# Kernel optimization log

Hardware: AMD Instinct MI355X
Metric: run time of the kernel (lower is better)

## Reference

```python
import jax, jax.numpy as jnp
import numpy as np


def setup_inputs() -> dict:
    key = jax.random.key(0)
    k1, k2, k3 = jax.random.split(key, 3)
    B, C, H, W = 8, 512, 32, 32
    x = jax.random.normal(k1, (B, C, H, W), dtype=jnp.float32)
    # Conv2d(ch, ch, 3, 1, 1) weights, PyTorch OIHW layout
    fan_in = C * 3 * 3
    weight = jax.random.normal(k2, (C, C, 3, 3), dtype=jnp.float32) / np.sqrt(fan_in)
    bias = jax.random.normal(k3, (C,), dtype=jnp.float32) * 0.01
    return {"x": x, "weight": weight, "bias": bias}


def reference(x, weight, bias):
    up = jnp.repeat(jnp.repeat(x, 2, axis=2), 2, axis=3)
    # Conv3x3, stride 1, padding 1 (same spatial size)
    out = jax.lax.conv_general_dilated(
        up, weight,
        window_strides=(1, 1),
        padding=((1, 1), (1, 1)),
        dimension_numbers=("NCHW", "OIHW", "NCHW"),
    )
    return out + bias[None, :, None, None]
```

## Files before the change

kernel.cpp:

```cpp
#include <hip/hip_runtime.h>
#include <hip/hip_bf16.h>
#include <stdint.h>


typedef __attribute__((ext_vector_type(8)))  __bf16 bf16x8;
typedef __attribute__((ext_vector_type(4)))  float  f32x4;
typedef __attribute__((ext_vector_type(4)))  int    int4v;

__device__ __forceinline__ void async16(const void* g, void* l) {
  __builtin_amdgcn_global_load_lds(
      (const __attribute__((address_space(1))) void*)g,
      (__attribute__((address_space(3))) void*)l,
      16, 0, 0);
}

__global__ void prep_weff(const float* __restrict__ w,
                          __hip_bfloat16* __restrict__ weff) {
  const int idx = blockIdx.x * 256 + threadIdx.x;
  const int co = idx >> 9;
  const int ci = idx & 511;
  const float* wp = w + (size_t)idx * 9;
  float t[9];
#pragma unroll
  for (int i = 0; i < 9; ++i) t[i] = wp[i];
#pragma unroll
  for (int py = 0; py < 2; ++py) {
#pragma unroll
    for (int px = 0; px < 2; ++px) {
      const int p = py * 2 + px;
#pragma unroll
      for (int ky = 0; ky < 2; ++ky) {
        const int ulo = (ky == 0) ? 0 : (py == 0 ? 1 : 2);
        const int uhi = (ky == 0) ? (py == 0 ? 0 : 1) : 2;
#pragma unroll
        for (int kx = 0; kx < 2; ++kx) {
          const int vlo = (kx == 0) ? 0 : (px == 0 ? 1 : 2);
          const int vhi = (kx == 0) ? (px == 0 ? 0 : 1) : 2;
          float s = 0.f;
          for (int u = ulo; u <= uhi; ++u)
            for (int v = vlo; v <= vhi; ++v)
              s += t[u * 3 + v];
          const int kk = ky * 2 + kx;
          weff[(((size_t)p * 512 + co) * 4 + kk) * 512 + ci] = __float2bfloat16(s);
        }
      }
    }
  }
}

__global__ void prep_xpad(const float* __restrict__ x,
                          __hip_bfloat16* __restrict__ xpad) {
  const int blk = blockIdx.x;
  const int cib = blk & 7;
  const int r   = (blk >> 3) & 31;
  const int b   = blk >> 8;
  const int tid = threadIdx.x;
  __shared__ __align__(16) __hip_bfloat16 ldsT[32][80];
  const int ci_l = tid >> 2;
  const int wq   = tid & 3;
  const float* xp = x + (((size_t)(b * 512 + cib * 64 + ci_l) * 32 + r) * 32) + wq * 8;
  float4 v0 = *(const float4*)(xp);
  float4 v1 = *(const float4*)(xp + 4);
  const int wb = wq * 8;
  ldsT[wb + 0][ci_l] = __float2bfloat16(v0.x);
  ldsT[wb + 1][ci_l] = __float2bfloat16(v0.y);
  ldsT[wb + 2][ci_l] = __float2bfloat16(v0.z);
  ldsT[wb + 3][ci_l] = __float2bfloat16(v0.w);
  ldsT[wb + 4][ci_l] = __float2bfloat16(v1.x);
  ldsT[wb + 5][ci_l] = __float2bfloat16(v1.y);
  ldsT[wb + 6][ci_l] = __float2bfloat16(v1.z);
  ldsT[wb + 7][ci_l] = __float2bfloat16(v1.w);
  __syncthreads();
  const int w_o = tid >> 3;
  const int ch  = tid & 7;
  char* dst = (char*)xpad +
      ((((size_t)(b * 34 + (r + 1)) * 34) + (w_o + 1)) * 512 + cib * 64 + ch * 8) * 2;
  *(int4v*)dst = *(const int4v*)&ldsT[w_o][ch * 8];
}

#define MM(a, b, c) __builtin_amdgcn_mfma_f32_16x16x32_bf16((a), (b), (c), 0, 0, 0)
#define BAR() asm volatile("s_barrier" ::: "memory")
#define PRIO(x) __builtin_amdgcn_s_setprio(x)
#define GATE(N) asm volatile("s_waitcnt vmcnt(" N ")" ::: "memory")

#define ST_A(T, h, d) do {                                                     \
    char* _l = lds + (d) * 32768 + (h) * 16384 + dA;                           \
    const __hip_bfloat16* _g = ((h) ? pA1 : pA0) + (size_t)(T) * 64;           \
    async16(_g, _l); async16(_g + 131072, _l + 8192); } while (0)

#define OFFB(T) (((((T) >> 4) * 34) + (((T) >> 3) & 1)) * 512 + ((T) & 7) * 64)
#define ST_B(T, h, d) do {                                                     \
    char* _l = lds + 65536 + (d) * 32768 + (h) * 16384 + dA;                   \
    const int _o = OFFB(T);                                                    \
    async16(((h) ? pB10 : pB00) + _o, _l);                                     \
    async16(((h) ? pB11 : pB01) + _o, _l + 8192); } while (0)

#define RD_A(D, S, mb) do {                                                    \
    _Pragma("unroll") for (int _m = 0; _m < 4; ++_m) {                         \
      (D)[_m * 2]     = *(const bf16x8*)((S) + ((mb) + _m) * 2048 + aoff0);    \
      (D)[_m * 2 + 1] = *(const bf16x8*)((S) + ((mb) + _m) * 2048 + aoff1); }  \
  } while (0)

#define RD_B(D, S, nb) do {                                                    \
    _Pragma("unroll") for (int _n = 0; _n < 2; ++_n) {                         \
      (D)[_n * 2]     = *(const bf16x8*)((S) + ((nb) + _n) * 2048 + aoff0);    \
      (D)[_n * 2 + 1] = *(const bf16x8*)((S) + ((nb) + _n) * 2048 + aoff1); }  \
  } while (0)

#define MFMAQ(mb, nb, A, B) do {                                               \
    _Pragma("unroll") for (int _m = 0; _m < 4; ++_m)                           \
      _Pragma("unroll") for (int _n = 0; _n < 2; ++_n) {                       \
        acc[(mb)+_m][(nb)+_n] = MM((A)[_m*2],   (B)[_n*2],   acc[(mb)+_m][(nb)+_n]); \
        acc[(mb)+_m][(nb)+_n] = MM((A)[_m*2+1], (B)[_n*2+1], acc[(mb)+_m][(nb)+_n]); } \
  } while (0)

#define ITER(T, SE, SM, S7, G3, G7) do {                                       \
                                                            \
  RD_A(A0, aS0, 0); RD_B(Bf, bS0, 0); if (SE) ST_A((T)+1, 1, 1);               \
  PRIO(1); MFMAQ(0, 0, A0, Bf); PRIO(0);                                       \
  RD_A(A1, aS0, 4); if (SE) ST_B((T)+1, 0, 1);                                 \
  PRIO(1); MFMAQ(4, 0, A1, Bf); PRIO(0);                                       \
  BAR();                                                                       \
                                                            \
  RD_B(Bf, bS0, 2); if (SE) ST_B((T)+1, 1, 1);                                 \
  PRIO(1); MFMAQ(4, 2, A1, Bf); PRIO(0);                                       \
  if (SM) ST_A((T)+2, 0, 0);                                                   \
  PRIO(1); MFMAQ(0, 2, A0, Bf); PRIO(0);                                       \
  GATE(G3); BAR();                                                             \
                                                            \
  RD_A(A0, aS1, 0); RD_B(Bf, bS1, 0); if (SM) ST_A((T)+2, 1, 0);               \
  PRIO(1); MFMAQ(0, 0, A0, Bf); PRIO(0);                                       \
  RD_A(A1, aS1, 4); if (SM) ST_B((T)+2, 0, 0);                                 \
  PRIO(1); MFMAQ(4, 0, A1, Bf); PRIO(0);                                       \
  BAR();                                                                       \
                                                            \
  RD_B(Bf, bS1, 2); if (SM) ST_B((T)+2, 1, 0);                                 \
  PRIO(1); MFMAQ(4, 2, A1, Bf); PRIO(0);                                       \
  if (S7) ST_A((T)+3, 0, 1);                                                   \
  PRIO(1); MFMAQ(0, 2, A0, Bf); PRIO(0);                                       \
  GATE(G7); BAR();                                                             \
} while (0)

__global__ __launch_bounds__(512, 2) void upconv_gemm(
    const __hip_bfloat16* __restrict__ xpad,
    const __hip_bfloat16* __restrict__ weff,
    const float* __restrict__ bias,
    float* __restrict__ out) {
  extern __shared__ __align__(16) char lds[];

  const int bid = blockIdx.x;
  const int g = bid & 7, i = bid >> 3;
  const int py = g >> 2;
  const int mt = (g >> 1) & 1;
  const int nh = g & 1;
  const int px = i & 1;
  const int nt = nh * 16 + (i >> 1);
  const int p  = py * 2 + px;
  const int co0 = mt << 8;
  const int n0  = nt << 8;
  const int b   = n0 >> 10;
  const int rb  = (n0 & 1023) >> 5;

  const int tid  = threadIdx.x;
  const int lane = tid & 63;
  const int wv   = tid >> 6;
  const int wr   = wv >> 2;
  const int wc   = wv & 3;

  const int srow = tid >> 3;
  const int sl   = (tid & 7) ^ (srow & 7);
  const int dA   = wv * 1024;

  const __hip_bfloat16* wpp = weff + ((size_t)p << 20);
  const __hip_bfloat16* pA0 = wpp + (size_t)(co0 + srow) * 2048 + sl * 8;
  const __hip_bfloat16* pA1 = pA0 + (size_t)128 * 2048;
  const __hip_bfloat16* pB00 = xpad +
      ((size_t)(b * 34 + rb + (srow >> 5) + py) * 34 + (srow & 31) + px) * 512 + sl * 8;
  const __hip_bfloat16* pB01 = xpad +
      ((size_t)(b * 34 + rb + ((64 + srow) >> 5) + py) * 34 + ((64 + srow) & 31) + px) * 512 + sl * 8;
  const __hip_bfloat16* pB10 = xpad +
      ((size_t)(b * 34 + rb + ((128 + srow) >> 5) + py) * 34 + ((128 + srow) & 31) + px) * 512 + sl * 8;
  const __hip_bfloat16* pB11 = xpad +
      ((size_t)(b * 34 + rb + ((192 + srow) >> 5) + py) * 34 + ((192 + srow) & 31) + px) * 512 + sl * 8;

  const int aoff0 = (lane & 15) * 128 + (((lane >> 4) ^ (lane & 7)) * 16);
  const int aoff1 = (lane & 15) * 128 + ((((lane >> 4) + 4) ^ (lane & 7)) * 16);
  const char* aS0 = lds + wr * 16384;
  const char* aS1 = aS0 + 32768;
  const char* bS0 = lds + 65536 + (wc >> 1) * 16384 + (wc & 1) * 8192;
  const char* bS1 = bS0 + 32768;

  f32x4 acc[8][4] = {};
  bf16x8 A0[8], A1[8], Bf[4];

  ST_A(0, 0, 0); ST_A(0, 1, 0); ST_B(0, 0, 0); ST_B(0, 1, 0);
  ST_A(1, 0, 1); ST_A(1, 1, 1); ST_B(1, 0, 1); ST_B(1, 1, 1);
  GATE("8"); BAR();

  ITER(0, false, true, true, "2", "2");
#pragma unroll 1
  for (int t = 2; t <= 28; t += 2) ITER(t, true, true, true, "2", "2");
  ITER(30, true, false, false, "0", "0");

#pragma unroll
  for (int m = 0; m < 8; ++m) {
    const int coB = co0 + wr * 128 + m * 16 + ((lane >> 4) << 2);
    float bv[4];
#pragma unroll
    for (int j = 0; j < 4; ++j) bv[j] = bias[coB + j];
#pragma unroll
    for (int nn = 0; nn < 4; ++nn) {
      const int nl = wc * 64 + nn * 16 + (lane & 15);
      const int rr = rb + (nl >> 5);
      const int ss = nl & 31;
      const int oh = rr * 2 + py;
      const int ow = ss * 2 + px;
      float* op = out + (((size_t)(b * 512 + coB) << 6) + oh) * 64 + ow;
#pragma unroll
      for (int j = 0; j < 4; ++j)
        op[(size_t)j * 4096] = acc[m][nn][j] + bv[j];
    }
  }
}

extern "C" void kernel_launch(void* const* d_in, const int* in_sizes, int n_in,
                              void* d_out, int out_size, void* d_ws, size_t ws_size,
                              hipStream_t stream) {
  (void)in_sizes; (void)n_in; (void)out_size; (void)ws_size;
  const float* x  = (const float*)d_in[0];
  const float* w  = (const float*)d_in[1];
  const float* bs = (const float*)d_in[2];
  float* out = (float*)d_out;
  char* ws = (char*)d_ws;
  __hip_bfloat16* xpad = (__hip_bfloat16*)ws;
  __hip_bfloat16* weff = (__hip_bfloat16*)(ws + (10u << 20));
  hipMemsetAsync(xpad, 0, (size_t)8 * 34 * 34 * 512 * 2, stream);
  prep_weff<<<dim3(1024), dim3(256), 0, stream>>>(w, weff);
  prep_xpad<<<dim3(2048), dim3(256), 0, stream>>>(x, xpad);
  upconv_gemm<<<dim3(256), dim3(512), 131072, stream>>>(xpad, weff, bs, out);
}
```

Baseline: 89.05 us.

## Double-buffer register fragments and coarsen global-to-LDS staging per barrier phase

Restructures the main loop so A and B fragments are double-buffered in registers (Aa/Ab, Ba/Bb), with LDS reads for the next quarter issued ahead of the MFMAs that consume the current one. Global-to-LDS async loads are merged into one A and one B issue per k-step instead of split halves, which changes the vmcnt gate values. The B pointers are now derived from a single base by fixed row offsets. The aim is to hide LDS read latency behind MFMAs, at the cost of more VGPRs, which could hurt occupancy at two blocks per CU.

New measurement: 84.26 us. 1.06x faster.

```diff
diff --git a/kernel.cpp b/kernel.cpp
--- a/kernel.cpp
+++ b/kernel.cpp
@@ -83,17 +83,20 @@
 #define PRIO(x) __builtin_amdgcn_s_setprio(x)
 #define GATE(N) asm volatile("s_waitcnt vmcnt(" N ")" ::: "memory")
 
-#define ST_A(T, h, d) do {                                                     \
-    char* _l = lds + (d) * 32768 + (h) * 16384 + dA;                           \
-    const __hip_bfloat16* _g = ((h) ? pA1 : pA0) + (size_t)(T) * 64;           \
-    async16(_g, _l); async16(_g + 131072, _l + 8192); } while (0)
+#define ST_A(T, d) do {                                                        \
+    char* _l = lds + (d) * 32768 + dA;                                         \
+    const __hip_bfloat16* _g = pA0 + (size_t)(T) * 64;                         \
+    async16(_g, _l); async16(_g + 131072, _l + 8192);                          \
+    async16(_g + 262144, _l + 16384); async16(_g + 393216, _l + 24576);        \
+  } while (0)
 
 #define OFFB(T) (((((T) >> 4) * 34) + (((T) >> 3) & 1)) * 512 + ((T) & 7) * 64)
-#define ST_B(T, h, d) do {                                                     \
-    char* _l = lds + 65536 + (d) * 32768 + (h) * 16384 + dA;                   \
+#define ST_B(T, d) do {                                                        \
+    char* _l = lds + 65536 + (d) * 32768 + dA;                                 \
     const int _o = OFFB(T);                                                    \
-    async16(((h) ? pB10 : pB00) + _o, _l);                                     \
-    async16(((h) ? pB11 : pB01) + _o, _l + 8192); } while (0)
+    async16(pB00 + _o, _l); async16(pB01 + _o, _l + 8192);                     \
+    async16(pB10 + _o, _l + 16384); async16(pB11 + _o, _l + 24576);            \
+  } while (0)
 
 #define RD_A(D, S, mb) do {                                                    \
     _Pragma("unroll") for (int _m = 0; _m < 4; ++_m) {                         \
@@ -114,31 +117,31 @@
         acc[(mb)+_m][(nb)+_n] = MM((A)[_m*2+1], (B)[_n*2+1], acc[(mb)+_m][(nb)+_n]); } \
   } while (0)
 
-#define ITER(T, SE, SM, S7, G3, G7) do {                                       \
-                                                            \
-  RD_A(A0, aS0, 0); RD_B(Bf, bS0, 0); if (SE) ST_A((T)+1, 1, 1);               \
-  PRIO(1); MFMAQ(0, 0, A0, Bf); PRIO(0);                                       \
-  RD_A(A1, aS0, 4); if (SE) ST_B((T)+1, 0, 1);                                 \
-  PRIO(1); MFMAQ(4, 0, A1, Bf); PRIO(0);                                       \
+#define ITER(T, SE, SO, GE, GO, LAST) do {                                     \
+                                                         \
+  RD_A(Ab, aS0, 4);                                                            \
+  PRIO(1); MFMAQ(0, 0, Aa, Ba); PRIO(0);                                       \
+  RD_B(Bb, bS0, 2);                                                            \
+  PRIO(1); MFMAQ(4, 0, Ab, Ba); PRIO(0);                                       \
   BAR();                                                                       \
-                                                            \
-  RD_B(Bf, bS0, 2); if (SE) ST_B((T)+1, 1, 1);                                 \
-  PRIO(1); MFMAQ(4, 2, A1, Bf); PRIO(0);                                       \
-  if (SM) ST_A((T)+2, 0, 0);                                                   \
-  PRIO(1); MFMAQ(0, 2, A0, Bf); PRIO(0);                                       \
-  GATE(G3); BAR();                                                             \
-                                                            \
-  RD_A(A0, aS1, 0); RD_B(Bf, bS1, 0); if (SM) ST_A((T)+2, 1, 0);               \
-  PRIO(1); MFMAQ(0, 0, A0, Bf); PRIO(0);                                       \
-  RD_A(A1, aS1, 4); if (SM) ST_B((T)+2, 0, 0);                                 \
-  PRIO(1); MFMAQ(4, 0, A1, Bf); PRIO(0);                                       \
+  if (SE) ST_A((T) + 2, 0);                                                    \
+  PRIO(1); MFMAQ(4, 2, Ab, Bb); PRIO(0);                                       \
+  GATE(GE); BAR();                                                             \
+  RD_A(Ab, aS1, 0); RD_B(Ba, bS1, 0);                                          \
+  if (SE) ST_B((T) + 2, 0);                                                    \
+  PRIO(1); MFMAQ(0, 2, Aa, Bb); PRIO(0);                                       \
+                                                          \
+  RD_A(Aa, aS1, 4);                                                            \
+  PRIO(1); MFMAQ(0, 0, Ab, Ba); PRIO(0);                                       \
+  RD_B(Bb, bS1, 2);                                                            \
+  PRIO(1); MFMAQ(4, 0, Aa, Ba); PRIO(0);                                       \
   BAR();                                                                       \
-                                                            \
-  RD_B(Bf, bS1, 2); if (SM) ST_B((T)+2, 1, 0);                                 \
-  PRIO(1); MFMAQ(4, 2, A1, Bf); PRIO(0);                                       \
-  if (S7) ST_A((T)+3, 0, 1);                                                   \
-  PRIO(1); MFMAQ(0, 2, A0, Bf); PRIO(0);                                       \
-  GATE(G7); BAR();                                                             \
+  if (SO) ST_A((T) + 3, 1);                                                    \
+  PRIO(1); MFMAQ(4, 2, Aa, Bb); PRIO(0);                                       \
+  GATE(GO); BAR();                                                             \
+  if (!LAST) { RD_A(Aa, aS0, 0); RD_B(Ba, bS0, 0); }                           \
+  if (SO) ST_B((T) + 3, 1);                                                    \
+  PRIO(1); MFMAQ(0, 2, Ab, Bb); PRIO(0);                                       \
 } while (0)
 
 __global__ __launch_bounds__(512, 2) void upconv_gemm(
@@ -173,15 +176,11 @@
 
   const __hip_bfloat16* wpp = weff + ((size_t)p << 20);
   const __hip_bfloat16* pA0 = wpp + (size_t)(co0 + srow) * 2048 + sl * 8;
-  const __hip_bfloat16* pA1 = pA0 + (size_t)128 * 2048;
   const __hip_bfloat16* pB00 = xpad +
       ((size_t)(b * 34 + rb + (srow >> 5) + py) * 34 + (srow & 31) + px) * 512 + sl * 8;
-  const __hip_bfloat16* pB01 = xpad +
-      ((size_t)(b * 34 + rb + ((64 + srow) >> 5) + py) * 34 + ((64 + srow) & 31) + px) * 512 + sl * 8;
-  const __hip_bfloat16* pB10 = xpad +
-      ((size_t)(b * 34 + rb + ((128 + srow) >> 5) + py) * 34 + ((128 + srow) & 31) + px) * 512 + sl * 8;
-  const __hip_bfloat16* pB11 = xpad +
-      ((size_t)(b * 34 + rb + ((192 + srow) >> 5) + py) * 34 + ((192 + srow) & 31) + px) * 512 + sl * 8;
+  const __hip_bfloat16* pB01 = pB00 + (size_t)2 * 34 * 512;
+  const __hip_bfloat16* pB10 = pB00 + (size_t)4 * 34 * 512;
+  const __hip_bfloat16* pB11 = pB00 + (size_t)6 * 34 * 512;
 
   const int aoff0 = (lane & 15) * 128 + (((lane >> 4) ^ (lane & 7)) * 16);
   const int aoff1 = (lane & 15) * 128 + ((((lane >> 4) + 4) ^ (lane & 7)) * 16);
@@ -191,16 +190,16 @@
   const char* bS1 = bS0 + 32768;
 
   f32x4 acc[8][4] = {};
-  bf16x8 A0[8], A1[8], Bf[4];
-
-  ST_A(0, 0, 0); ST_A(0, 1, 0); ST_B(0, 0, 0); ST_B(0, 1, 0);
-  ST_A(1, 0, 1); ST_A(1, 1, 1); ST_B(1, 0, 1); ST_B(1, 1, 1);
+  bf16x8 Aa[8], Ab[8], Ba[4], Bb[4];
+
+  ST_A(0, 0); ST_B(0, 0);
+  ST_A(1, 1); ST_B(1, 1);
   GATE("8"); BAR();
-
-  ITER(0, false, true, true, "2", "2");
+  RD_A(Aa, aS0, 0); RD_B(Ba, bS0, 0);
+
 #pragma unroll 1
-  for (int t = 2; t <= 28; t += 2) ITER(t, true, true, true, "2", "2");
-  ITER(30, true, false, false, "0", "0");
+  for (int t = 0; t <= 28; t += 2) ITER(t, true, true, "4", "4", false);
+  ITER(30, false, false, "0", "0", true);
 
 #pragma unroll
   for (int m = 0; m < 8; ++m) {
```
